# Kernel optimization log

Hardware: AMD Instinct MI355X
Metric: run time of the kernel (lower is better)

## Reference

```python
import jax, jax.numpy as jnp
import numpy as np

B, T, N, D = 8, 512, 64, 128
PRED, HEADS, HID = 96, 8, 256
KERNELS = (17, 49)
NUM_LAYERS = 1
NUM_BLOCKS = 1
IDX_T = np.arange(64)   # lowest 64 of T//2=256 rfft modes (mode_select='low')
IDX_C = np.arange(32)   # min(modes, (N+1)//2)=32 lowest channel-frequency modes


def _mov_avg(x, k):
    # x: [B, T, N]; replicate-pad (k-1)//2 on both ends, then box filter (AvgPool1d stride 1)
    pad = (k - 1) // 2
    xp = jnp.concatenate([jnp.repeat(x[:, :1], pad, axis=1), x, jnp.repeat(x[:, -1:], pad, axis=1)], axis=1)
    c = jnp.cumsum(xp, axis=1)
    c = jnp.concatenate([jnp.zeros_like(c[:, :1]), c], axis=1)
    return (c[:, k:] - c[:, :-k]) / k


def _decomp_multi(x, dec_w, dec_b):
    # series_decomp_multi: softmax-weighted mixture of moving averages
    mm = jnp.stack([_mov_avg(x, k) for k in KERNELS], axis=-1)        # [B,T,N,K]
    w = jax.nn.softmax(x[..., None] * dec_w + dec_b, axis=-1)         # Linear(1,K) on x, softmax over K
    trend = jnp.sum(mm * w, axis=-1)
    return x - trend, trend


def _complex_attn(x, Wq, Wk, Wv, Wo):
    # x: complex64 [B, L, M, D]; multi-head attention over the M selected frequency modes.
    # Real projection weights applied to complex activations; attention weights are
    # softmax over |q k^H| / sqrt(dh); values stay complex.
    Bq, L, M, Dm = x.shape
    dh = Dm // HEADS
    q = jnp.einsum('blmd,de->blme', x, Wq).reshape(Bq, L, M, HEADS, dh)
    k = jnp.einsum('blmd,de->blme', x, Wk).reshape(Bq, L, M, HEADS, dh)
    v = jnp.einsum('blmd,de->blme', x, Wv).reshape(Bq, L, M, HEADS, dh)
    s = jnp.einsum('blmhd,blnhd->blhmn', q, jnp.conj(k))              # complex scores
    w = jax.nn.softmax(jnp.abs(s) / np.sqrt(dh), axis=-1)             # real attn weights
    o = jnp.einsum('blhmn,blnhd->blmhd', w.astype(x.dtype), v).reshape(Bq, L, M, Dm)
    return jnp.einsum('blmd,de->blme', o, Wo)


def _cem(x, Wq, Wk, Wv, Wo):
    # channel-frequency attention; x: [B, N, T, D]
    xp = jnp.transpose(x, (0, 2, 1, 3))                               # [B,T,N,D]
    xf = jnp.fft.rfft(xp, axis=2)                                     # [B,T,N//2+1,D]
    xs = xf[:, :, IDX_C, :]                                           # gather selected modes
    for _ in range(NUM_LAYERS):
        xs = _complex_attn(xs, Wq, Wk, Wv, Wo)
    yf = jnp.zeros((x.shape[0], T, N // 2 + 1, D), dtype=xf.dtype).at[:, :, IDX_C, :].set(xs)
    y = jnp.fft.irfft(yf, n=N, axis=2)
    return jnp.transpose(y, (0, 2, 1, 3))


def _tem(x, Wq, Wk, Wv, Wo):
    # temporal-frequency attention; x: [B, N, T, D]
    xf = jnp.fft.rfft(x, axis=2)                                      # [B,N,T//2+1,D]
    xs = xf[:, :, IDX_T, :]
    for _ in range(NUM_LAYERS):
        xs = _complex_attn(xs, Wq, Wk, Wv, Wo)
    yf = jnp.zeros((x.shape[0], N, T // 2 + 1, D), dtype=xf.dtype).at[:, :, IDX_T, :].set(xs)
    return jnp.fft.irfft(yf, n=T, axis=2)


def setup_inputs() -> dict:
    key = jax.random.key(0)
    ks = jax.random.split(key, 24)
    r = lambda i, shape, s: jax.random.normal(ks[i], shape, jnp.float32) * s
    K = len(KERNELS)
    return {
        'x': jax.random.normal(ks[0], (B, T, N), jnp.float32),
        'embeddings': jax.random.normal(ks[1], (1, D), jnp.float32),
        'dec_w': r(2, (K,), 1.0),
        'dec_b': jnp.zeros((K,), jnp.float32),
        'mlp_w1': r(3, (T, HID), 1.0 / np.sqrt(T)),
        'mlp_b1': jnp.zeros((HID,), jnp.float32),
        'mlp_w2': r(4, (HID, HID), 1.0 / np.sqrt(HID)),
        'mlp_b2': jnp.zeros((HID,), jnp.float32),
        'mlp_w3': r(5, (HID, PRED), 1.0 / np.sqrt(HID)),
        'mlp_b3': jnp.zeros((PRED,), jnp.float32),
        'cem_Wq': r(6, (D, D), 0.02), 'cem_Wk': r(7, (D, D), 0.02),
        'cem_Wv': r(8, (D, D), 0.02), 'cem_Wo': r(9, (D, D), 0.02),
        'tem_Wq': r(10, (D, D), 0.02), 'tem_Wk': r(11, (D, D), 0.02),
        'tem_Wv': r(12, (D, D), 0.02), 'tem_Wo': r(13, (D, D), 0.02),
        'dr_w': r(14, (D, 1), 1.0 / np.sqrt(D)),
        'dr_b': jnp.zeros((1,), jnp.float32),
        'out_w': r(15, (T, PRED), 1.0 / np.sqrt(T)),
        'out_b': jnp.zeros((PRED,), jnp.float32),
        'W_fuse': jnp.ones((2,), jnp.float32),
    }


def reference(x, embeddings, dec_w, dec_b, mlp_w1, mlp_b1, mlp_w2, mlp_b2, mlp_w3, mlp_b3,
              cem_Wq, cem_Wk, cem_Wv, cem_Wo, tem_Wq, tem_Wk, tem_Wv, tem_Wo,
              dr_w, dr_b, out_w, out_b, W_fuse):
    res, trend = _decomp_multi(x, dec_w, dec_b)
    t = jnp.transpose(trend, (0, 2, 1))                               # [B,N,T]
    h = jax.nn.relu(t @ mlp_w1 + mlp_b1)
    h = jax.nn.relu(h @ mlp_w2 + mlp_b2)
    trend_out = jnp.transpose(h @ mlp_w3 + mlp_b3, (0, 2, 1))         # [B,PRED,N]
    # tokenEmb: [B,T,N] -> [B,N,T,1] * [1,D]
    xe = jnp.transpose(res, (0, 2, 1))[..., None] * embeddings[0]      # [B,N,T,D]
    for _ in range(NUM_BLOCKS):
        xe = _cem(xe, cem_Wq, cem_Wk, cem_Wv, cem_Wo)
    for _ in range(NUM_BLOCKS):
        xe = _tem(xe, tem_Wq, tem_Wk, tem_Wv, tem_Wo)
    xr = jnp.einsum('bntd,do->bnto', xe, dr_w)[..., 0] + dr_b[0]      # dim_reduction -> [B,N,T]
    xo = jnp.transpose(jnp.einsum('bnt,tp->bnp', xr, out_w) + out_b, (0, 2, 1))  # [B,PRED,N]
    return W_fuse[0] * xo + W_fuse[1] * trend_out
```

## Files before the change

### kernel.cpp

```cpp
#include <hip/hip_runtime.h>
#include <hip/hip_bf16.h>

typedef __hip_bfloat16 bf16;
typedef float v2f __attribute__((ext_vector_type(2)));

constexpr int CB = 8;
constexpr int CT = 512;
constexpr int CN = 64;
constexpr int CD = 128;
constexpr int CP = 96;
constexpr int CH = 8;
constexpr int CDH = 16;
constexpr int CHID = 256;
constexpr int CM = 32;
constexpr int CG = 64;
constexpr float TWO_PI = 6.28318530717958647692f;

__device__ __forceinline__ float LD(const void* p, size_t i, bool f) {
  return f ? ((const float*)p)[i] : __bfloat162float(((const bf16*)p)[i]);
}
template <bool F32>
__device__ __forceinline__ float LDT(const void* p, size_t i) {
  return F32 ? ((const float*)p)[i] : __bfloat162float(((const bf16*)p)[i]);
}

__device__ __forceinline__ bool detect_f32(const void* x) {
  const unsigned int* xw = (const unsigned int*)x;
  unsigned int w = xw[threadIdx.x & 63];
  unsigned int e = (w >> 7) & 0xFF;
  unsigned long long m = __ballot(e >= 0x90 || e <= 0x60);
  return __popcll(m) > 3;
}

struct MArgs {
  const void *x, *dec_w, *dec_b, *out_w, *emb, *cWq, *cWk, *cWv, *cWo;
  const void *tWq, *tWk, *tWv, *tWo, *drw, *drb, *out_b, *wfuse;
  const void *w1, *b1, *w2, *b2, *w3, *b3;
  float *trendo, *Pbuf, *ewq, *ewk, *ewv, *wod, *owr, *owi, *chg;
  void* out;
};

__global__ __launch_bounds__(256, 4) void kPre(MArgs a) {
  __shared__ float sm[512];
  float* eml = sm;
  float* pp = sm + 128;
  float* prod = sm + 384;
  bool f32 = detect_f32(a.x);
  int tid = threadIdx.x;
  if (tid < 128) eml[tid] = LD(a.emb, tid, f32);
  __syncthreads();
  {
    int e = tid & 127, which = tid >> 7;
    const void* Wm = which ? a.cWk : a.cWq;
    float p = 0.f;
    #pragma unroll 8
    for (int d = 0; d < CD; ++d) p = fmaf(eml[d], LD(Wm, (size_t)d * CD + e, f32), p);
    pp[which * 128 + e] = p;
  }
  __syncthreads();
  if (tid < 128) prod[tid] = pp[tid] * pp[128 + tid];
  __syncthreads();
  if (tid < CH) {
    float s = 0.f;
    #pragma unroll
    for (int j = 0; j < 16; ++j) s += prod[tid * 16 + j];
    a.chg[tid] = fabsf(s);
  }
}

template <bool F32>
__device__ void k2_body(float* sm, const MArgs& a) {
  float* xbuf = sm;
  float* rows = sm;
  float* h1 = sm + 1536;
  float* h2 = sm + 2048;
  int r0 = blockIdx.x * 2;
  int b = r0 >> 6, n0 = r0 & 63;
  int tid = threadIdx.x;
  size_t xb = (size_t)b * CT * CN + n0;
  for (int i = tid; i < CT * 2; i += 256) {
    int t = i >> 1, q = i & 1;
    xbuf[t * 3 + q] = LDT<F32>(a.x, xb + (size_t)t * CN + q);
  }
  __syncthreads();
  float trv[4];
  int q = tid & 1, tl = tid >> 1, t0 = tl * 4;
  {
    float w0 = LDT<F32>(a.dec_w, 0), w1 = LDT<F32>(a.dec_w, 1);
    float c0 = LDT<F32>(a.dec_b, 0), c1 = LDT<F32>(a.dec_b, 1);
    float s17 = 0.f, s49 = 0.f;
    #pragma unroll
    for (int o = -8; o <= 8; ++o) {
      int u = t0 + o; u = u < 0 ? 0 : (u > CT - 1 ? CT - 1 : u);
      s17 += xbuf[u * 3 + q];
    }
    #pragma unroll
    for (int o = -24; o <= 24; ++o) {
      int u = t0 + o; u = u < 0 ? 0 : (u > CT - 1 ? CT - 1 : u);
      s49 += xbuf[u * 3 + q];
    }
    #pragma unroll
    for (int k = 0; k < 4; ++k) {
      int t = t0 + k;
      if (k > 0) {
        int up8 = t + 8 > CT - 1 ? CT - 1 : t + 8;
        int dn9 = t - 9 < 0 ? 0 : t - 9;
        int up24 = t + 24 > CT - 1 ? CT - 1 : t + 24;
        int dn25 = t - 25 < 0 ? 0 : t - 25;
        s17 += xbuf[up8 * 3 + q] - xbuf[dn9 * 3 + q];
        s49 += xbuf[up24 * 3 + q] - xbuf[dn25 * 3 + q];
      }
      float m0 = s17 * (1.f / 17.f), m1 = s49 * (1.f / 49.f);
      float xv = xbuf[t * 3 + q];
      float l0 = xv * w0 + c0, l1 = xv * w1 + c1;
      float mx = fmaxf(l0, l1);
      float e0 = __expf(l0 - mx), e1 = __expf(l1 - mx);
      trv[k] = (e0 * m0 + e1 * m1) / (e0 + e1);
    }
  }
  __syncthreads();
  #pragma unroll
  for (int k = 0; k < 4; ++k) rows[q * CT + t0 + k] = trv[k];
  __syncthreads();
  int c = tid;
  float a0, a1;
  {
    float bias = LDT<F32>(a.b1, c);
    a0 = a1 = 0.f;
    #pragma unroll 16
    for (int t = 0; t < CT; ++t) {
      float w = LDT<F32>(a.w1, t * CHID + c);
      a0 = fmaf(rows[t], w, a0);
      a1 = fmaf(rows[CT + t], w, a1);
    }
    h1[c] = fmaxf(a0 + bias, 0.f);
    h1[CHID + c] = fmaxf(a1 + bias, 0.f);
  }
  __syncthreads();
  {
    float bias = LDT<F32>(a.b2, c);
    a0 = a1 = 0.f;
    #pragma unroll 16
    for (int i = 0; i < CHID; ++i) {
      float w = LDT<F32>(a.w2, i * CHID + c);
      a0 = fmaf(h1[i], w, a0);
      a1 = fmaf(h1[CHID + i], w, a1);
    }
    h2[c] = fmaxf(a0 + bias, 0.f);
    h2[CHID + c] = fmaxf(a1 + bias, 0.f);
  }
  __syncthreads();
  if (tid < 2 * CP) {
    int p = tid < CP ? tid : tid - CP;
    int qh = tid < CP ? 0 : 1;
    float bias = LDT<F32>(a.b3, p);
    a0 = 0.f;
    #pragma unroll 16
    for (int i = 0; i < CHID; ++i)
      a0 = fmaf(h2[qh * CHID + i], LDT<F32>(a.w3, i * CP + p), a0);
    a.trendo[((size_t)(b * CN + n0 + qh)) * CP + p] = a0 + bias;
  }
}

__global__ __launch_bounds__(256, 4) void kS2(MArgs a) {
  __shared__ __align__(16) float sm[4608];
  bool f32 = detect_f32(a.x);
  int blk = blockIdx.x, tid = threadIdx.x;
  if (blk < 256) {
    if (f32) k2_body<true>(sm, a);
    else     k2_body<false>(sm, a);
  } else if (blk < 1280) {
    float* xl = sm;
    float2* SL = (float2*)sm;
    float* rowl = sm + 3328;
    float* Rr = sm + 3584;
    float* Ri = sm + 3712;
    float* aR = sm + 3840;
    float* chl = sm + 4096;
    int bk = blk - 256;
    int b = bk >> 7, tbase = (bk & 127) * 4;
    int w = tid >> 6, lane = tid & 63;
    size_t xb = (size_t)b * CT * CN;
    for (int i = tid; i < 52 * 64; i += 256) {
      int r = i >> 6, n = i & 63;
      int u = tbase - 24 + r; u = u < 0 ? 0 : (u > CT - 1 ? CT - 1 : u);
      xl[i] = LD(a.x, xb + (size_t)u * CN + n, f32);
    }
    if (tid < CH) chl[tid] = a.chg[tid];
    __syncthreads();
    {
      int Lt = 24 + w;
      float w0 = LD(a.dec_w, 0, f32), w1 = LD(a.dec_w, 1, f32);
      float c0 = LD(a.dec_b, 0, f32), c1 = LD(a.dec_b, 1, f32);
      const float* xc = xl + Lt * 64 + lane;
      float pa = 0.f, pb = 0.f;
      #pragma unroll
      for (int o = -8; o <= 8; o += 2) pa += xc[o * 64];
      #pragma unroll
      for (int o = -7; o <= 7; o += 2) pb += xc[o * 64];
      float s17 = pa + pb;
      float qa = 0.f, qb = 0.f;
      #pragma unroll
      for (int o = 9; o <= 23; o += 2) qa += xc[o * 64] + xc[-o * 64];
      #pragma unroll
      for (int o = 10; o <= 24; o += 2) qb += xc[o * 64] + xc[-o * 64];
      float s49 = s17 + qa + qb;
      float m0 = s17 * (1.f / 17.f), m1 = s49 * (1.f / 49.f);
      float xv = xc[0];
      float l0 = xv * w0 + c0, l1 = xv * w1 + c1;
      float mx = fmaxf(l0, l1);
      float e0 = __expf(l0 - mx), e1 = __expf(l1 - mx);
      float tr = (e0 * m0 + e1 * m1) / (e0 + e1);
      rowl[w * 64 + lane] = xv - tr;
    }
    __syncthreads();
    float am, amax;
    {
      int m = lane & 31, half = lane >> 5;
      float cf, sf;
      sincosf((float)m * (TWO_PI / CN), &sf, &cf);
      float wr = (half & m & 1) ? -1.f : 1.f, wi = 0.f;
      float rr = 0.f, ri = 0.f;
      const float* rw = rowl + w * 64 + half * 32;
      #pragma unroll 8
      for (int j = 0; j < 32; ++j) {
        float xv = rw[j];
        rr = fmaf(xv, wr, rr);
        ri = fmaf(-xv, wi, ri);
        float nr = wr * cf - wi * sf; wi = wi * cf + wr * sf; wr = nr;
      }
      rr += __shfl_xor(rr, 32);
      ri += __shfl_xor(ri, 32);
      am = sqrtf(rr * rr + ri * ri);
      if (half == 0) { Rr[w * 32 + m] = rr; Ri[w * 32 + m] = ri; aR[w * 32 + m] = am; }
      amax = am;
      #pragma unroll
      for (int s2 = 1; s2 < 32; s2 <<= 1) amax = fmaxf(amax, __shfl_xor(amax, s2));
    }
    __syncthreads();
    {
      float base2 = 0.25f * 1.44269504f * am;
      int hb = lane >> 5;
      float al0 = chl[hb] * base2;
      float al1 = chl[hb + 2] * base2;
      float al2 = chl[hb + 4] * base2;
      float al3 = chl[hb + 6] * base2;
      float den0 = 0, sr0 = 0, si0 = 0, den1 = 0, sr1 = 0, si1 = 0;
      float den2 = 0, sr2 = 0, si2 = 0, den3 = 0, sr3 = 0, si3 = 0;
      const float* aRw = aR + w * 32;
      const float* Rrw = Rr + w * 32;
      const float* Riw = Ri + w * 32;
      for (int n2 = 0; n2 < CM; ++n2) {
        float d = aRw[n2] - amax;
        float rrn = Rrw[n2], rin = Riw[n2];
        float e0 = exp2f(al0 * d); den0 += e0; sr0 = fmaf(e0, rrn, sr0); si0 = fmaf(e0, rin, si0);
        float e1 = exp2f(al1 * d); den1 += e1; sr1 = fmaf(e1, rrn, sr1); si1 = fmaf(e1, rin, si1);
        float e2 = exp2f(al2 * d); den2 += e2; sr2 = fmaf(e2, rrn, sr2); si2 = fmaf(e2, rin, si2);
        float e3 = exp2f(al3 * d); den3 += e3; sr3 = fmaf(e3, rrn, sr3); si3 = fmaf(e3, rin, si3);
      }
      float r0 = 1.f / den0, r1 = 1.f / den1, r2 = 1.f / den2, r3 = 1.f / den3;
      SL[w * 256 + lane      ] = make_float2(sr0 * r0, si0 * r0);
      SL[w * 256 + lane + 64 ] = make_float2(sr1 * r1, si1 * r1);
      SL[w * 256 + lane + 128] = make_float2(sr2 * r2, si2 * r2);
      SL[w * 256 + lane + 192] = make_float2(sr3 * r3, si3 * r3);
    }
    __syncthreads();
    {
      int n2 = lane;
      const float2* Sw = SL + w * 256;
      float cd, sd;
      sincosf((float)n2 * (TWO_PI / CN), &sd, &cd);
      float c2 = cd * cd - sd * sd, s2 = 2.f * sd * cd;
      float pxA = 1.f, pyA = 0.f;
      float acc[8];
      #pragma unroll
      for (int h = 0; h < CH; ++h) acc[h] = -Sw[h * 32].x;
      for (int f2 = 0; f2 < 16; ++f2) {
        float pxB = pxA * cd - pyA * sd, pyB = pyA * cd + pxA * sd;
        float px2A = pxA + pxA, ny2A = -(pyA + pyA);
        float px2B = pxB + pxB, ny2B = -(pyB + pyB);
        #pragma unroll
        for (int h = 0; h < CH; ++h) {
          float4 sv = *(const float4*)(Sw + h * 32 + f2 * 2);
          acc[h] = fmaf(sv.x, px2A, acc[h]);
          acc[h] = fmaf(sv.y, ny2A, acc[h]);
          acc[h] = fmaf(sv.z, px2B, acc[h]);
          acc[h] = fmaf(sv.w, ny2B, acc[h]);
        }
        float nx = pxA * c2 - pyA * s2; pyA = pyA * c2 + pxA * s2; pxA = nx;
      }
      int t = tbase + w;
      float* Pb = a.Pbuf + (((size_t)(b * CN + n2)) * CT + t) * CH;
      ((float4*)Pb)[0] = make_float4(acc[0] * (1.f / CN), acc[1] * (1.f / CN),
                                     acc[2] * (1.f / CN), acc[3] * (1.f / CN));
      ((float4*)Pb)[1] = make_float4(acc[4] * (1.f / CN), acc[5] * (1.f / CN),
                                     acc[6] * (1.f / CN), acc[7] * (1.f / CN));
    }
  } else if (blk < 1344) {
    float* ps = sm;
    int g = blk - 1280;
    int tc = tid >> 7, idx = tid & 127;
    if (idx < CP) {
      int p = idx, t0 = tc * 256;
      float s0, c0v, ss, cs;
      sincosf((float)((g * t0) & (CT - 1)) * (TWO_PI / CT), &s0, &c0v);
      sincosf((float)g * (TWO_PI / CT), &ss, &cs);
      float wr = c0v, wi = s0, ar = 0.f, ai = 0.f;
      #pragma unroll 16
      for (int t = 0; t < 256; ++t) {
        float w = LD(a.out_w, (size_t)(t0 + t) * CP + p, f32);
        ar = fmaf(w, wr, ar); ai = fmaf(w, wi, ai);
        float nr = wr * cs - wi * ss; wi = wi * cs + wr * ss; wr = nr;
      }
      ps[(tc * CP + p) * 2] = ar; ps[(tc * CP + p) * 2 + 1] = ai;
    }
    __syncthreads();
    if (tid < CP) {
      a.owr[g * CP + tid] = ps[tid * 2] + ps[(CP + tid) * 2];
      a.owi[g * CP + tid] = ps[tid * 2 + 1] + ps[(CP + tid) * 2 + 1];
    }
  } else if (blk < 1356) {
    float* eml = sm;
    float* evl = sm + 128;
    float* ewoh = sm + 160;
    int bi = blk - 1344;
    int half = tid >> 7, e = tid & 127;
    int pairIdx = bi * 2 + half;
    int which = pairIdx >> 3, h = pairIdx & 7;
    if (tid < 128) eml[tid] = LD(a.emb, tid, f32);
    __syncthreads();
    if (e < 16) {
      float acc = 0;
      #pragma unroll 8
      for (int d = 0; d < CD; ++d) acc += eml[d] * LD(a.cWv, d * CD + h * CDH + e, f32);
      evl[half * 16 + e] = acc;
    }
    __syncthreads();
    {
      float acc = 0;
      #pragma unroll
      for (int j = 0; j < CDH; ++j)
        acc += evl[half * 16 + j] * LD(a.cWo, (h * CDH + j) * CD + e, f32);
      ewoh[half * 128 + e] = acc;
    }
    __syncthreads();
    {
      const void* W = which == 0 ? a.tWq : (which == 1 ? a.tWk : a.tWv);
      float acc = 0;
      #pragma unroll 8
      for (int d = 0; d < CD; ++d) acc += ewoh[half * 128 + d] * LD(W, d * CD + e, f32);
      (which == 0 ? a.ewq : (which == 1 ? a.ewk : a.ewv))[h * CD + e] = acc;
    }
  } else {
    float* drl = sm;
    if (tid < 128) drl[tid] = LD(a.drw, tid, f32);
    __syncthreads();
    if (tid < 128) {
      float acc = 0;
      #pragma unroll 8
      for (int d = 0; d < CD; ++d) acc += LD(a.tWo, tid * CD + d, f32) * drl[d];
      a.wod[tid] = acc;
    }
  }
}

__global__ __launch_bounds__(512, 4) void kC(MArgs a) {
  __shared__ __align__(16) float sm[13504];
  float* Pl = sm;
  float* QL = sm + 4352;
  float* Cl = sm + 5632;
  float* Ul = sm + 6144;
  float2* vdL = (float2*)(sm + 6208);
  float2* zL = (float2*)(sm + 7232);
  float* zrow = sm + 8256;
  float* Ab = sm + 8384;
  bool f32 = detect_f32(a.x);
  int blk = blockIdx.x, tid = threadIdx.x;
  int b = blk >> 6, n = blk & 63;
  const float4* src4 = (const float4*)(a.Pbuf + ((size_t)(b * CN + n)) * CT * CH);
  for (int i = tid; i < 1024; i += 512) {
    float4 v = src4[i];
    int t = i >> 1, half = i & 1;
    int k = t >> 6, u = t & 63;
    float* dst = Pl + u * 68 + half * 32 + k;
    dst[0] = v.x; dst[8] = v.y; dst[16] = v.z; dst[24] = v.w;
  }
  for (int id = tid; id < 512 + 64; id += 512) {
    if (id < 512) {
      int h = id >> 6, aa = (id >> 3) & 7, b2 = id & 7;
      float c = 0;
      #pragma unroll
      for (int j = 0; j < CDH; ++j)
        c += a.ewq[aa * CD + h * CDH + j] * a.ewk[b2 * CD + h * CDH + j];
      Cl[id] = c;
    } else {
      int r = id - 512;
      int h = r >> 3, aa = r & 7;
      float c = 0;
      #pragma unroll
      for (int j = 0; j < CDH; ++j) c += a.ewv[aa * CD + h * CDH + j] * a.wod[h * CDH + j];
      Ul[r] = c;
    }
  }
  __syncthreads();
  {
    int u = tid >> 3, h = tid & 7;
    const float* pr = Pl + u * 68 + h * 8;
    float p0 = pr[0], p1 = pr[1], p2 = pr[2], p3 = pr[3];
    float p4 = pr[4], p5 = pr[5], p6 = pr[6], p7 = pr[7];
    const float s = 0.70710678118654752f;
    float p04a = p0 + p4, p04s = p0 - p4;
    float p26a = p2 + p6, p26s = p2 - p6;
    float p17a = p1 + p7, p17s = p1 - p7;
    float p35a = p3 + p5, p35s = p3 - p5;
    float e1 = s * (p17a - p35a);
    float e2 = s * (p17s + p35s);
    float* ab = Ab + u * 80 + h * 10;
    ab[0] = p04a + p26a + p17a + p35a;
    ab[1] = 0.f;
    ab[2] = p04s + e1;
    ab[3] = -e2 - p26s;
    ab[4] = p04a - p26a;
    ab[5] = -(p17s - p35s);
    ab[6] = p04s - e1;
    ab[7] = -e2 + p26s;
    ab[8] = (p04a + p26a) - (p17a + p35a);
    ab[9] = 0.f;
  }
  __syncthreads();
  {
    int g = tid >> 3, h = tid & 7;
    int rho = g & 7;
    int rc = rho < 5 ? rho : 8 - rho;
    float ncsgn = rho < 5 ? -1.f : 1.f;
    float cs, sn;
    sincosf((float)g * (TWO_PI / CT), &sn, &cs);
    v2f wv = {1.f, 0.f};
    v2f qv = {0.f, 0.f};
    const float2* ab = (const float2*)(Ab + h * 10 + rc * 2);
    #pragma unroll 4
    for (int u = 0; u < 64; ++u) {
      float2 A = ab[u * 40];
      float are = A.x, naim = ncsgn * A.y;
      v2f ws = {wv.y, -wv.x};
      qv += (v2f){are, are} * wv;
      qv += (v2f){naim, naim} * ws;
      wv = (v2f){cs, cs} * wv + (v2f){sn, sn} * ws;
    }
    QL[g * 20 + h * 2] = qv.x;
    QL[g * 20 + h * 2 + 1] = qv.y;
  }
  __syncthreads();
  int h = tid >> 6, m = tid & 63;
  v2f qp[8];
  {
    const float4* q4 = (const float4*)(QL + m * 20);
    #pragma unroll
    for (int j = 0; j < 4; ++j) {
      float4 qv = q4[j];
      qp[2 * j]     = (v2f){qv.x, qv.y};
      qp[2 * j + 1] = (v2f){qv.z, qv.w};
    }
  }
  {
    float vr = 0, vi = 0;
    #pragma unroll
    for (int aa = 0; aa < 8; ++aa) {
      float u = Ul[h * 8 + aa];
      vr = fmaf(qp[aa].x, u, vr); vi = fmaf(qp[aa].y, u, vi);
    }
    vdL[h * 64 + m] = make_float2(vr, vi);
  }
  v2f uu[8], vv[8];
  #pragma unroll
  for (int bb = 0; bb < 8; ++bb) {
    v2f acc = {0.f, 0.f};
    #pragma unroll
    for (int aa = 0; aa < 8; ++aa) acc += qp[aa] * Cl[(h * 8 + aa) * 8 + bb];
    uu[bb] = acc;
    vv[bb] = (v2f){acc.y, -acc.x};
  }
  float mx = -1e30f, den = 0.f, zr = 0.f, zi = 0.f;
  #pragma unroll 4
  for (int g = 0; g < CG; ++g) {
    const float4* y4 = (const float4*)(QL + g * 20);
    v2f sr2 = {0.f, 0.f}, si2 = {0.f, 0.f};
    #pragma unroll
    for (int j = 0; j < 4; ++j) {
      float4 yv = y4[j];
      v2f ya = {yv.x, yv.y}, yb = {yv.z, yv.w};
      sr2 = uu[2 * j] * ya + sr2;
      si2 = vv[2 * j] * ya + si2;
      sr2 = uu[2 * j + 1] * yb + sr2;
      si2 = vv[2 * j + 1] * yb + si2;
    }
    float sr = sr2.x + sr2.y;
    float si = si2.x + si2.y;
    float s = 0.25f * sqrtf(sr * sr + si * si);
    if (s > mx) {
      float f = __expf(mx - s);
      den *= f; zr *= f; zi *= f; mx = s;
    }
    float e = __expf(s - mx);
    float2 vd = vdL[h * 64 + g];
    den += e; zr = fmaf(e, vd.x, zr); zi = fmaf(e, vd.y, zi);
  }
  {
    float rv = 1.f / den;
    zL[h * 64 + m] = make_float2(zr * rv, zi * rv);
  }
  __syncthreads();
  if (tid < 128) {
    int g = tid >> 1, c = tid & 1;
    float acc = 0;
    #pragma unroll
    for (int hh = 0; hh < CH; ++hh) acc += c ? zL[hh * 64 + g].y : zL[hh * 64 + g].x;
    zrow[g * 2 + c] = acc;
  }
  __syncthreads();
  if (tid < CP) {
    int p = tid;
    float acc = zrow[0] * a.owr[p] - zrow[1] * a.owi[p];
    #pragma unroll 8
    for (int g = 1; g < CG; ++g)
      acc += 2.f * (zrow[g * 2] * a.owr[g * CP + p] - zrow[g * 2 + 1] * a.owi[g * CP + p]);
    float xo = acc * (1.f / CT) + LD(a.drb, 0, f32) * a.owr[p] + LD(a.out_b, p, f32);
    float val = LD(a.wfuse, 0, f32) * xo
              + LD(a.wfuse, 1, f32) * a.trendo[((size_t)(b * CN + n)) * CP + p];
    size_t oidx = ((size_t)(b * CP + p)) * CN + n;
    if (f32) ((float*)a.out)[oidx] = val;
    else ((bf16*)a.out)[oidx] = __float2bfloat16(val);
  }
}

extern "C" void kernel_launch(void* const* d_in, const int* in_sizes, int n_in,
                              void* d_out, int out_size, void* d_ws, size_t ws_size,
                              hipStream_t stream) {
  float* W = (float*)d_ws;
  MArgs a;
  a.x = d_in[0];   a.emb = d_in[1];  a.dec_w = d_in[2]; a.dec_b = d_in[3];
  a.w1 = d_in[4];  a.b1 = d_in[5];   a.w2 = d_in[6];    a.b2 = d_in[7];
  a.w3 = d_in[8];  a.b3 = d_in[9];
  a.cWq = d_in[10]; a.cWk = d_in[11]; a.cWv = d_in[12]; a.cWo = d_in[13];
  a.tWq = d_in[14]; a.tWk = d_in[15]; a.tWv = d_in[16]; a.tWo = d_in[17];
  a.drw = d_in[18]; a.drb = d_in[19]; a.out_w = d_in[20]; a.out_b = d_in[21];
  a.wfuse = d_in[22];
  a.trendo = W; W += (size_t)CB * CN * CP;
  a.Pbuf = W;   W += (size_t)CB * CN * CT * CH;
  a.ewq = W;    W += CH * CD;
  a.ewk = W;    W += CH * CD;
  a.ewv = W;    W += CH * CD;
  a.wod = W;    W += CD;
  a.owr = W;    W += CG * CP;
  a.owi = W;    W += CG * CP;
  a.chg = W;    W += CH;
  a.out = d_out;

  kPre<<<1, 256, 0, stream>>>(a);
  kS2<<<1357, 256, 0, stream>>>(a);
  kC<<<512, 512, 0, stream>>>(a);
}
```

Baseline: 185.3 us.

## Vectorize trend MLP weight loads with split-K partials and drop redundant barriers

```diff
diff --git a/kernel.cpp b/kernel.cpp
--- a/kernel.cpp
+++ b/kernel.cpp
@@ -23,6 +23,9 @@
 __device__ __forceinline__ float LDT(const void* p, size_t i) {
   return F32 ? ((const float*)p)[i] : __bfloat162float(((const bf16*)p)[i]);
 }
+__device__ __forceinline__ float b2f(short s) {
+  return __uint_as_float(((unsigned int)(unsigned short)s) << 16);
+}
 
 __device__ __forceinline__ bool detect_f32(const void* x) {
   const unsigned int* xw = (const unsigned int*)x;
@@ -74,6 +77,7 @@
   float* rows = sm;
   float* h1 = sm + 1536;
   float* h2 = sm + 2048;
+  float* part = sm + 2560;
   int r0 = blockIdx.x * 2;
   int b = r0 >> 6, n0 = r0 & 63;
   int tid = threadIdx.x;
@@ -122,39 +126,94 @@
   #pragma unroll
   for (int k = 0; k < 4; ++k) rows[q * CT + t0 + k] = trv[k];
   __syncthreads();
-  int c = tid;
-  float a0, a1;
-  {
+  int tt = tid >> 6, cq = tid & 63;
+  {
+    float ac0 = 0, ac1 = 0, ac2 = 0, ac3 = 0, ac4 = 0, ac5 = 0, ac6 = 0, ac7 = 0;
+    int tg = tt * 128;
+    if (F32) {
+      const float4* w4 = (const float4*)a.w1;
+      #pragma unroll 8
+      for (int t = tg; t < tg + 128; ++t) {
+        float4 wv = w4[t * 64 + cq];
+        float rA = rows[t], rB = rows[CT + t];
+        ac0 = fmaf(rA, wv.x, ac0); ac1 = fmaf(rA, wv.y, ac1);
+        ac2 = fmaf(rA, wv.z, ac2); ac3 = fmaf(rA, wv.w, ac3);
+        ac4 = fmaf(rB, wv.x, ac4); ac5 = fmaf(rB, wv.y, ac5);
+        ac6 = fmaf(rB, wv.z, ac6); ac7 = fmaf(rB, wv.w, ac7);
+      }
+    } else {
+      const short4* w4 = (const short4*)a.w1;
+      #pragma unroll 8
+      for (int t = tg; t < tg + 128; ++t) {
+        short4 sv = w4[t * 64 + cq];
+        float wx = b2f(sv.x), wy = b2f(sv.y), wz = b2f(sv.z), ww = b2f(sv.w);
+        float rA = rows[t], rB = rows[CT + t];
+        ac0 = fmaf(rA, wx, ac0); ac1 = fmaf(rA, wy, ac1);
+        ac2 = fmaf(rA, wz, ac2); ac3 = fmaf(rA, ww, ac3);
+        ac4 = fmaf(rB, wx, ac4); ac5 = fmaf(rB, wy, ac5);
+        ac6 = fmaf(rB, wz, ac6); ac7 = fmaf(rB, ww, ac7);
+      }
+    }
+    float4* pp = (float4*)(part + tt * 512 + cq * 4);
+    pp[0] = make_float4(ac0, ac1, ac2, ac3);
+    pp[64] = make_float4(ac4, ac5, ac6, ac7);
+  }
+  __syncthreads();
+  {
+    int c = tid;
     float bias = LDT<F32>(a.b1, c);
-    a0 = a1 = 0.f;
-    #pragma unroll 16
-    for (int t = 0; t < CT; ++t) {
-      float w = LDT<F32>(a.w1, t * CHID + c);
-      a0 = fmaf(rows[t], w, a0);
-      a1 = fmaf(rows[CT + t], w, a1);
-    }
-    h1[c] = fmaxf(a0 + bias, 0.f);
-    h1[CHID + c] = fmaxf(a1 + bias, 0.f);
-  }
-  __syncthreads();
-  {
+    float s0 = part[c] + part[512 + c] + part[1024 + c] + part[1536 + c];
+    float s1 = part[256 + c] + part[768 + c] + part[1280 + c] + part[1792 + c];
+    h1[c] = fmaxf(s0 + bias, 0.f);
+    h1[CHID + c] = fmaxf(s1 + bias, 0.f);
+  }
+  __syncthreads();
+  {
+    float ac0 = 0, ac1 = 0, ac2 = 0, ac3 = 0, ac4 = 0, ac5 = 0, ac6 = 0, ac7 = 0;
+    int ig = tt * 64;
+    if (F32) {
+      const float4* w4 = (const float4*)a.w2;
+      #pragma unroll 8
+      for (int i = ig; i < ig + 64; ++i) {
+        float4 wv = w4[i * 64 + cq];
+        float rA = h1[i], rB = h1[CHID + i];
+        ac0 = fmaf(rA, wv.x, ac0); ac1 = fmaf(rA, wv.y, ac1);
+        ac2 = fmaf(rA, wv.z, ac2); ac3 = fmaf(rA, wv.w, ac3);
+        ac4 = fmaf(rB, wv.x, ac4); ac5 = fmaf(rB, wv.y, ac5);
+        ac6 = fmaf(rB, wv.z, ac6); ac7 = fmaf(rB, wv.w, ac7);
+      }
+    } else {
+      const short4* w4 = (const short4*)a.w2;
+      #pragma unroll 8
+      for (int i = ig; i < ig + 64; ++i) {
+        short4 sv = w4[i * 64 + cq];
+        float wx = b2f(sv.x), wy = b2f(sv.y), wz = b2f(sv.z), ww = b2f(sv.w);
+        float rA = h1[i], rB = h1[CHID + i];
+        ac0 = fmaf(rA, wx, ac0); ac1 = fmaf(rA, wy, ac1);
+        ac2 = fmaf(rA, wz, ac2); ac3 = fmaf(rA, ww, ac3);
+        ac4 = fmaf(rB, wx, ac4); ac5 = fmaf(rB, wy, ac5);
+        ac6 = fmaf(rB, wz, ac6); ac7 = fmaf(rB, ww, ac7);
+      }
+    }
+    float4* pp = (float4*)(part + tt * 512 + cq * 4);
+    pp[0] = make_float4(ac0, ac1, ac2, ac3);
+    pp[64] = make_float4(ac4, ac5, ac6, ac7);
+  }
+  __syncthreads();
+  {
+    int c = tid;
     float bias = LDT<F32>(a.b2, c);
-    a0 = a1 = 0.f;
-    #pragma unroll 16
-    for (int i = 0; i < CHID; ++i) {
-      float w = LDT<F32>(a.w2, i * CHID + c);
-      a0 = fmaf(h1[i], w, a0);
-      a1 = fmaf(h1[CHID + i], w, a1);
-    }
-    h2[c] = fmaxf(a0 + bias, 0.f);
-    h2[CHID + c] = fmaxf(a1 + bias, 0.f);
+    float s0 = part[c] + part[512 + c] + part[1024 + c] + part[1536 + c];
+    float s1 = part[256 + c] + part[768 + c] + part[1280 + c] + part[1792 + c];
+    h2[c] = fmaxf(s0 + bias, 0.f);
+    h2[CHID + c] = fmaxf(s1 + bias, 0.f);
   }
   __syncthreads();
   if (tid < 2 * CP) {
     int p = tid < CP ? tid : tid - CP;
     int qh = tid < CP ? 0 : 1;
     float bias = LDT<F32>(a.b3, p);
-    a0 = 0.f;
+    float a0 = 0.f;
     #pragma unroll 16
     for (int i = 0; i < CHID; ++i)
       a0 = fmaf(h2[qh * CHID + i], LDT<F32>(a.w3, i * CP + p), a0);
@@ -237,7 +296,6 @@
       #pragma unroll
       for (int s2 = 1; s2 < 32; s2 <<= 1) amax = fmaxf(amax, __shfl_xor(amax, s2));
     }
-    __syncthreads();
     {
       float base2 = 0.25f * 1.44269504f * am;
       int hb = lane >> 5;
@@ -264,7 +322,6 @@
       SL[w * 256 + lane + 128] = make_float2(sr2 * r2, si2 * r2);
       SL[w * 256 + lane + 192] = make_float2(sr3 * r3, si3 * r3);
     }
-    __syncthreads();
     {
       int n2 = lane;
       const float2* Sw = SL + w * 256;
```

Measured after the change: 183.5 us. Within noise of the previous version (-1.0%).
